# Performance work log

Measured on AMD Instinct MI355X. Metric: run time of the kernel, lower is better.

The kernel has to match this reference:

```python
import jax, jax.numpy as jnp
import numpy as np

N = 1_000_000   # gaussians
K_NB = 10       # neighbor control points per gaussian
K_TOTAL = 300   # num_fine control points


def _normalize(q, eps=1e-8):
    return q / jnp.maximum(jnp.linalg.norm(q, axis=-1, keepdims=True), eps)


def quaternion_to_rotation_matrix(q):
    # q: [..., 4] in (w, x, y, z); normalized before conversion
    q = _normalize(q)
    w, x, y, z = q[..., 0], q[..., 1], q[..., 2], q[..., 3]
    R = jnp.stack([
        jnp.stack([1 - 2 * (y * y + z * z), 2 * (x * y - w * z), 2 * (x * z + w * y)], axis=-1),
        jnp.stack([2 * (x * y + w * z), 1 - 2 * (x * x + z * z), 2 * (y * z - w * x)], axis=-1),
        jnp.stack([2 * (x * z - w * y), 2 * (y * z + w * x), 1 - 2 * (x * x + y * y)], axis=-1),
    ], axis=-2)  # [..., 3, 3]
    return R


def quaternion_multiply(a, b):
    # Hamilton product, (w, x, y, z)
    aw, ax, ay, az = a[..., 0], a[..., 1], a[..., 2], a[..., 3]
    bw, bx, by, bz = b[..., 0], b[..., 1], b[..., 2], b[..., 3]
    return jnp.stack([
        aw * bw - ax * bx - ay * by - az * bz,
        aw * bx + ax * bw + ay * bz - az * by,
        aw * by - ax * bz + ay * bw + az * bx,
        aw * bz + ax * by - ay * bx + az * bw,
    ], axis=-1)


def setup_inputs() -> dict:
    key = jax.random.key(0)
    ks = jax.random.split(key, 7)
    means = jax.random.normal(ks[0], (N, 3), dtype=jnp.float32)
    quaternions = _normalize(jax.random.normal(ks[1], (N, 4), dtype=jnp.float32))
    w = jax.random.uniform(ks[2], (N, K_NB), dtype=jnp.float32) + 1e-3
    weights = w / w.sum(-1, keepdims=True)  # blending weights sum to 1
    indices = jax.random.randint(ks[3], (N, K_NB), 0, K_TOTAL)
    ctrl_translations = 0.1 * jax.random.normal(ks[4], (K_TOTAL, 3), dtype=jnp.float32)
    ctrl_rotations = _normalize(jax.random.normal(ks[5], (K_TOTAL, 4), dtype=jnp.float32))
    ctrl_positions = jax.random.normal(ks[6], (K_TOTAL, 3), dtype=jnp.float32)
    return {
        'means': means, 'quaternions': quaternions, 'weights': weights,
        'ctrl_translations': ctrl_translations, 'ctrl_rotations': ctrl_rotations,
        'ctrl_positions': ctrl_positions, 'indices': indices,
    }


def reference(means, quaternions, weights, ctrl_translations, ctrl_rotations, ctrl_positions, indices):
    # gather neighbor control-point transforms
    nb_trans = ctrl_translations[indices]   # [N, K, 3]
    nb_rots = ctrl_rotations[indices]       # [N, K, 4]
    nb_pos = ctrl_positions[indices]        # [N, K, 3]

    diff = means[:, None, :] - nb_pos                       # [N, K, 3]
    R_ctrl = quaternion_to_rotation_matrix(nb_rots)         # [N, K, 3, 3]
    rotated_diff = jnp.einsum('nkij,nkj->nki', R_ctrl, diff)
    deformed_per_cp = rotated_diff + nb_pos + nb_trans      # [N, K, 3]

    w = weights[..., None]                                  # [N, K, 1]
    deformed_means = (w * deformed_per_cp).sum(axis=1)      # [N, 3]

    blended_rot = _normalize((w * nb_rots).sum(axis=1))     # [N, 4]
    deformed_quats = quaternion_multiply(blended_rot, quaternions)
    return deformed_means, deformed_quats
```

## Files before the change

### kernel.cpp

```cpp
#include <hip/hip_runtime.h>
#include <math.h>


struct Accum {
    float W;
    float Mxx, Myy, Mzz, Mxy, Mxz, Myz, Mwx, Mwy, Mwz;
    float qsw, qsx, qsy, qsz;
    float bsx, bsy, bsz;
};

__device__ __forceinline__ void acc_init(Accum& a) {
    a.W = 0.0f;
    a.Mxx = a.Myy = a.Mzz = 0.0f;
    a.Mxy = a.Mxz = a.Myz = 0.0f;
    a.Mwx = a.Mwy = a.Mwz = 0.0f;
    a.qsw = a.qsx = a.qsy = a.qsz = 0.0f;
    a.bsx = a.bsy = a.bsz = 0.0f;
}

__device__ __forceinline__ void acc_neighbor(Accum& a, const float4* __restrict__ tbl,
                                             int K_TOTAL, int cp, float w) {
    float4 q = tbl[cp];
    float4 b = tbl[K_TOTAL + cp];
    float tw = w * q.x, tx = w * q.y, ty = w * q.z, tz = w * q.w;
    a.W += w;
    a.Mxx = fmaf(tx, q.y, a.Mxx);
    a.Myy = fmaf(ty, q.z, a.Myy);
    a.Mzz = fmaf(tz, q.w, a.Mzz);
    a.Mxy = fmaf(tx, q.z, a.Mxy);
    a.Mxz = fmaf(tx, q.w, a.Mxz);
    a.Myz = fmaf(ty, q.w, a.Myz);
    a.Mwx = fmaf(tw, q.y, a.Mwx);
    a.Mwy = fmaf(tw, q.z, a.Mwy);
    a.Mwz = fmaf(tw, q.w, a.Mwz);
    a.qsw += tw; a.qsx += tx; a.qsy += ty; a.qsz += tz;
    a.bsx = fmaf(w, b.x, a.bsx);
    a.bsy = fmaf(w, b.y, a.bsy);
    a.bsz = fmaf(w, b.z, a.bsz);
}

__device__ __forceinline__ void acc_epilogue(const Accum& a,
                                             float mx, float my, float mz,
                                             float4 g,
                                             float* dmx, float* dmy, float* dmz,
                                             float4* oq) {
    float A00 = a.W - 2.0f * (a.Myy + a.Mzz);
    float A01 = 2.0f * (a.Mxy - a.Mwz);
    float A02 = 2.0f * (a.Mxz + a.Mwy);
    float A10 = 2.0f * (a.Mxy + a.Mwz);
    float A11 = a.W - 2.0f * (a.Mxx + a.Mzz);
    float A12 = 2.0f * (a.Myz - a.Mwx);
    float A20 = 2.0f * (a.Mxz - a.Mwy);
    float A21 = 2.0f * (a.Myz + a.Mwx);
    float A22 = a.W - 2.0f * (a.Mxx + a.Myy);

    *dmx = fmaf(A00, mx, fmaf(A01, my, fmaf(A02, mz, a.bsx)));
    *dmy = fmaf(A10, mx, fmaf(A11, my, fmaf(A12, mz, a.bsy)));
    *dmz = fmaf(A20, mx, fmaf(A21, my, fmaf(A22, mz, a.bsz)));

    float n   = sqrtf(a.qsw * a.qsw + a.qsx * a.qsx + a.qsy * a.qsy + a.qsz * a.qsz);
    float inv = 1.0f / fmaxf(n, 1e-8f);
    float bw = a.qsw * inv, bx = a.qsx * inv, by = a.qsy * inv, bz = a.qsz * inv;

    float gw = g.x, gx = g.y, gy = g.z, gz = g.w;
    oq->x = bw * gw - bx * gx - by * gy - bz * gz;
    oq->y = bw * gx + bx * gw + by * gz - bz * gy;
    oq->z = bw * gy - bx * gz + by * gw + bz * gx;
    oq->w = bw * gz + bx * gy - by * gx + bz * gw;
}

__device__ __forceinline__ void build_table(
    const float* __restrict__ ctrl_trans,
    const float* __restrict__ ctrl_rot,
    const float* __restrict__ ctrl_pos,
    float4* __restrict__ tbl, int K_TOTAL)
{
    for (int cp = threadIdx.x; cp < K_TOTAL; cp += blockDim.x) {
        float4 qv = ((const float4*)ctrl_rot)[cp];
        float qw = qv.x, qx = qv.y, qy = qv.z, qz = qv.w;
        float nn  = sqrtf(qw * qw + qx * qx + qy * qy + qz * qz);
        float inv = 1.0f / fmaxf(nn, 1e-8f);
        float w = qw * inv, x = qx * inv, y = qy * inv, z = qz * inv;
        float R00 = 1.0f - 2.0f * (y * y + z * z);
        float R01 = 2.0f * (x * y - w * z);
        float R02 = 2.0f * (x * z + w * y);
        float R10 = 2.0f * (x * y + w * z);
        float R11 = 1.0f - 2.0f * (x * x + z * z);
        float R12 = 2.0f * (y * z - w * x);
        float R20 = 2.0f * (x * z - w * y);
        float R21 = 2.0f * (y * z + w * x);
        float R22 = 1.0f - 2.0f * (x * x + y * y);
        float px = ctrl_pos[cp * 3 + 0];
        float py = ctrl_pos[cp * 3 + 1];
        float pz = ctrl_pos[cp * 3 + 2];
        float tx = ctrl_trans[cp * 3 + 0];
        float ty = ctrl_trans[cp * 3 + 1];
        float tz = ctrl_trans[cp * 3 + 2];
        tbl[cp]           = make_float4(w, x, y, z);
        tbl[K_TOTAL + cp] = make_float4(px + tx - (R00 * px + R01 * py + R02 * pz),
                                        py + ty - (R10 * px + R11 * py + R12 * pz),
                                        pz + tz - (R20 * px + R21 * py + R22 * pz),
                                        0.0f);
    }
}

__global__ __launch_bounds__(256) void deform_stage_kernel(
    const float* __restrict__ means,
    const float* __restrict__ quats,
    const float* __restrict__ weights,
    const float* __restrict__ ctrl_trans,
    const float* __restrict__ ctrl_rot,
    const float* __restrict__ ctrl_pos,
    const int*   __restrict__ indices,
    float* __restrict__ out_means,
    float* __restrict__ out_quats,
    int N, int K_TOTAL)
{
    extern __shared__ float smem[];
    float4* tbl  = (float4*)smem;
    float*  sIdx = smem + 8 * K_TOTAL;
    float*  sW   = sIdx + 2560;

    const int t = threadIdx.x;
    const long long blockBase = (long long)blockIdx.x * 256;
    const long long fbase = blockBase * 10;
    const long long ftot  = (long long)N * 10;

#pragma unroll
    for (int j = t; j < 640; j += 256) {
        long long f0 = fbase + 4LL * j;
        float4 vi, vw;
        if (f0 + 3 < ftot) {
            vi = ((const float4*)indices)[f0 / 4];
            vw = ((const float4*)weights)[f0 / 4];
        } else {
            float ei[4], ew[4];
#pragma unroll
            for (int e = 0; e < 4; e++) {
                long long f = f0 + e;
                bool ok = f < ftot;
                ei[e] = ok ? ((const float*)indices)[f] : 0.0f;
                ew[e] = ok ? weights[f] : 0.0f;
            }
            vi = make_float4(ei[0], ei[1], ei[2], ei[3]);
            vw = make_float4(ew[0], ew[1], ew[2], ew[3]);
        }
        *(float4*)(sIdx + 4 * j) = vi;
        *(float4*)(sW   + 4 * j) = vw;
    }

    build_table(ctrl_trans, ctrl_rot, ctrl_pos, tbl, K_TOTAL);

    __syncthreads();

    long long g = blockBase + t;
    if (g >= N) return;

    const int2*   ip2 = (const int2*)  (sIdx + t * 10);
    const float2* wp2 = (const float2*)(sW   + t * 10);
    int2   i01 = ip2[0], i23 = ip2[1], i45 = ip2[2], i67 = ip2[3], i89 = ip2[4];
    float2 w01 = wp2[0], w23 = wp2[1], w45 = wp2[2], w67 = wp2[3], w89 = wp2[4];

    float mx = means[g * 3 + 0];
    float my = means[g * 3 + 1];
    float mz = means[g * 3 + 2];
    float4 gq = ((const float4*)quats)[g];

    Accum a; acc_init(a);
    acc_neighbor(a, tbl, K_TOTAL, i01.x, w01.x);
    acc_neighbor(a, tbl, K_TOTAL, i01.y, w01.y);
    acc_neighbor(a, tbl, K_TOTAL, i23.x, w23.x);
    acc_neighbor(a, tbl, K_TOTAL, i23.y, w23.y);
    acc_neighbor(a, tbl, K_TOTAL, i45.x, w45.x);
    acc_neighbor(a, tbl, K_TOTAL, i45.y, w45.y);
    acc_neighbor(a, tbl, K_TOTAL, i67.x, w67.x);
    acc_neighbor(a, tbl, K_TOTAL, i67.y, w67.y);
    acc_neighbor(a, tbl, K_TOTAL, i89.x, w89.x);
    acc_neighbor(a, tbl, K_TOTAL, i89.y, w89.y);

    float dx, dy, dz;
    float4 oq;
    acc_epilogue(a, mx, my, mz, gq, &dx, &dy, &dz, &oq);

    out_means[g * 3 + 0] = dx;
    out_means[g * 3 + 1] = dy;
    out_means[g * 3 + 2] = dz;
    ((float4*)out_quats)[g] = oq;
}

__global__ __launch_bounds__(256) void deform_generic_kernel(
    const float* __restrict__ means,
    const float* __restrict__ quats,
    const float* __restrict__ weights,
    const float* __restrict__ ctrl_trans,
    const float* __restrict__ ctrl_rot,
    const float* __restrict__ ctrl_pos,
    const int*   __restrict__ indices,
    float* __restrict__ out_means,
    float* __restrict__ out_quats,
    int N, int K_NB, int K_TOTAL)
{
    extern __shared__ float smem[];
    float4* tbl = (float4*)smem;
    build_table(ctrl_trans, ctrl_rot, ctrl_pos, tbl, K_TOTAL);
    __syncthreads();

    long long i = (long long)blockIdx.x * blockDim.x + threadIdx.x;
    if (i >= N) return;

    const int*   idx_row = indices + i * K_NB;
    const float* w_row   = weights + i * K_NB;
    Accum a; acc_init(a);
    for (int k = 0; k < K_NB; k++)
        acc_neighbor(a, tbl, K_TOTAL, idx_row[k], w_row[k]);

    float mx = means[i * 3 + 0];
    float my = means[i * 3 + 1];
    float mz = means[i * 3 + 2];
    float4 gq = ((const float4*)quats)[i];
    float dx, dy, dz;
    float4 oq;
    acc_epilogue(a, mx, my, mz, gq, &dx, &dy, &dz, &oq);
    out_means[i * 3 + 0] = dx;
    out_means[i * 3 + 1] = dy;
    out_means[i * 3 + 2] = dz;
    ((float4*)out_quats)[i] = oq;
}

extern "C" void kernel_launch(void* const* d_in, const int* in_sizes, int n_in,
                              void* d_out, int out_size, void* d_ws, size_t ws_size,
                              hipStream_t stream) {
    const float* means      = (const float*)d_in[0];
    const float* quats      = (const float*)d_in[1];
    const float* weights    = (const float*)d_in[2];
    const float* ctrl_trans = (const float*)d_in[3];
    const float* ctrl_rot   = (const float*)d_in[4];
    const float* ctrl_pos   = (const float*)d_in[5];
    const int*   indices    = (const int*)d_in[6];

    int N       = in_sizes[0] / 3;
    int K_NB    = in_sizes[2] / N;
    int K_TOTAL = in_sizes[3] / 3;

    float* out_means = (float*)d_out;
    float* out_quats = (float*)d_out + (long long)N * 3;

    int block = 256;
    int grid  = (int)(((long long)N + block - 1) / block);

    if (K_NB == 10) {
        size_t smem = (size_t)(8 * K_TOTAL + 5120) * sizeof(float);
        deform_stage_kernel<<<grid, block, smem, stream>>>(
            means, quats, weights, ctrl_trans, ctrl_rot, ctrl_pos, indices,
            out_means, out_quats, N, K_TOTAL);
    } else {
        size_t smem = (size_t)K_TOTAL * 2 * sizeof(float4);
        deform_generic_kernel<<<grid, block, smem, stream>>>(
            means, quats, weights, ctrl_trans, ctrl_rot, ctrl_pos, indices,
            out_means, out_quats, N, K_NB, K_TOTAL);
    }
}
```

Before: 148.8 us.

## Replace smem-staged kernel with persistent grid-stride kernel and register prefetch

Replaces the per-block kernel that staged indices and weights through shared memory with a persistent grid-stride kernel capped at 1024 blocks. Each thread loads the next element's indices, weights, mean and quaternion into registers while it processes the current one. The control-point table is now built once per persistent block instead of once per 256 elements. The trade-offs are uncoalesced strided loads of indices and weights (40-byte rows per thread), higher register pressure from the double-buffered data, and a grid size that may not give enough waves in flight.

```diff
diff --git a/kernel.cpp b/kernel.cpp
--- a/kernel.cpp
+++ b/kernel.cpp
@@ -104,7 +104,57 @@
     }
 }
 
-__global__ __launch_bounds__(256) void deform_stage_kernel(
+struct GData {
+    int2   i01, i23, i45, i67, i89;
+    float2 w01, w23, w45, w67, w89;
+    float  mx, my, mz;
+    float4 gq;
+};
+
+__device__ __forceinline__ void load_g(
+    const float* __restrict__ means,
+    const float* __restrict__ quats,
+    const float* __restrict__ weights,
+    const int*   __restrict__ indices,
+    long long g, GData& d)
+{
+    const int2*   ip = (const int2*)(indices + g * 10);
+    const float2* wp = (const float2*)(weights + g * 10);
+    d.i01 = ip[0]; d.i23 = ip[1]; d.i45 = ip[2]; d.i67 = ip[3]; d.i89 = ip[4];
+    d.w01 = wp[0]; d.w23 = wp[1]; d.w45 = wp[2]; d.w67 = wp[3]; d.w89 = wp[4];
+    d.mx = means[g * 3 + 0];
+    d.my = means[g * 3 + 1];
+    d.mz = means[g * 3 + 2];
+    d.gq = ((const float4*)quats)[g];
+}
+
+__device__ __forceinline__ void process_g(
+    const float4* __restrict__ tbl, int K_TOTAL, const GData& d,
+    long long g, float* __restrict__ out_means, float* __restrict__ out_quats)
+{
+    Accum a; acc_init(a);
+    acc_neighbor(a, tbl, K_TOTAL, d.i01.x, d.w01.x);
+    acc_neighbor(a, tbl, K_TOTAL, d.i01.y, d.w01.y);
+    acc_neighbor(a, tbl, K_TOTAL, d.i23.x, d.w23.x);
+    acc_neighbor(a, tbl, K_TOTAL, d.i23.y, d.w23.y);
+    acc_neighbor(a, tbl, K_TOTAL, d.i45.x, d.w45.x);
+    acc_neighbor(a, tbl, K_TOTAL, d.i45.y, d.w45.y);
+    acc_neighbor(a, tbl, K_TOTAL, d.i67.x, d.w67.x);
+    acc_neighbor(a, tbl, K_TOTAL, d.i67.y, d.w67.y);
+    acc_neighbor(a, tbl, K_TOTAL, d.i89.x, d.w89.x);
+    acc_neighbor(a, tbl, K_TOTAL, d.i89.y, d.w89.y);
+
+    float dx, dy, dz;
+    float4 oq;
+    acc_epilogue(a, d.mx, d.my, d.mz, d.gq, &dx, &dy, &dz, &oq);
+
+    out_means[g * 3 + 0] = dx;
+    out_means[g * 3 + 1] = dy;
+    out_means[g * 3 + 2] = dz;
+    ((float4*)out_quats)[g] = oq;
+}
+
+__global__ __launch_bounds__(256) void deform_pipe_kernel(
     const float* __restrict__ means,
     const float* __restrict__ quats,
     const float* __restrict__ weights,
@@ -116,76 +166,32 @@
     float* __restrict__ out_quats,
     int N, int K_TOTAL)
 {
-    extern __shared__ float smem[];
-    float4* tbl  = (float4*)smem;
-    float*  sIdx = smem + 8 * K_TOTAL;
-    float*  sW   = sIdx + 2560;
-
-    const int t = threadIdx.x;
-    const long long blockBase = (long long)blockIdx.x * 256;
-    const long long fbase = blockBase * 10;
-    const long long ftot  = (long long)N * 10;
-
-#pragma unroll
-    for (int j = t; j < 640; j += 256) {
-        long long f0 = fbase + 4LL * j;
-        float4 vi, vw;
-        if (f0 + 3 < ftot) {
-            vi = ((const float4*)indices)[f0 / 4];
-            vw = ((const float4*)weights)[f0 / 4];
-        } else {
-            float ei[4], ew[4];
-#pragma unroll
-            for (int e = 0; e < 4; e++) {
-                long long f = f0 + e;
-                bool ok = f < ftot;
-                ei[e] = ok ? ((const float*)indices)[f] : 0.0f;
-                ew[e] = ok ? weights[f] : 0.0f;
-            }
-            vi = make_float4(ei[0], ei[1], ei[2], ei[3]);
-            vw = make_float4(ew[0], ew[1], ew[2], ew[3]);
+    extern __shared__ float4 tbl[];
+    build_table(ctrl_trans, ctrl_rot, ctrl_pos, tbl, K_TOTAL);
+    __syncthreads();
+
+    const long long stride = (long long)gridDim.x * blockDim.x;
+    long long g = (long long)blockIdx.x * blockDim.x + threadIdx.x;
+    if (g >= N) return;
+
+    GData cur;
+    load_g(means, quats, weights, indices, g, cur);
+
+    for (;;) {
+        long long gn = g + stride;
+        bool have_next = gn < N;
+
+        GData nxt;
+        if (have_next) {
+            load_g(means, quats, weights, indices, gn, nxt);
         }
-        *(float4*)(sIdx + 4 * j) = vi;
-        *(float4*)(sW   + 4 * j) = vw;
+
+        process_g(tbl, K_TOTAL, cur, g, out_means, out_quats);
+
+        if (!have_next) break;
+        cur = nxt;
+        g = gn;
     }
-
-    build_table(ctrl_trans, ctrl_rot, ctrl_pos, tbl, K_TOTAL);
-
-    __syncthreads();
-
-    long long g = blockBase + t;
-    if (g >= N) return;
-
-    const int2*   ip2 = (const int2*)  (sIdx + t * 10);
-    const float2* wp2 = (const float2*)(sW   + t * 10);
-    int2   i01 = ip2[0], i23 = ip2[1], i45 = ip2[2], i67 = ip2[3], i89 = ip2[4];
-    float2 w01 = wp2[0], w23 = wp2[1], w45 = wp2[2], w67 = wp2[3], w89 = wp2[4];
-
-    float mx = means[g * 3 + 0];
-    float my = means[g * 3 + 1];
-    float mz = means[g * 3 + 2];
-    float4 gq = ((const float4*)quats)[g];
-
-    Accum a; acc_init(a);
-    acc_neighbor(a, tbl, K_TOTAL, i01.x, w01.x);
-    acc_neighbor(a, tbl, K_TOTAL, i01.y, w01.y);
-    acc_neighbor(a, tbl, K_TOTAL, i23.x, w23.x);
-    acc_neighbor(a, tbl, K_TOTAL, i23.y, w23.y);
-    acc_neighbor(a, tbl, K_TOTAL, i45.x, w45.x);
-    acc_neighbor(a, tbl, K_TOTAL, i45.y, w45.y);
-    acc_neighbor(a, tbl, K_TOTAL, i67.x, w67.x);
-    acc_neighbor(a, tbl, K_TOTAL, i67.y, w67.y);
-    acc_neighbor(a, tbl, K_TOTAL, i89.x, w89.x);
-    acc_neighbor(a, tbl, K_TOTAL, i89.y, w89.y);
-
-    float dx, dy, dz;
-    float4 oq;
-    acc_epilogue(a, mx, my, mz, gq, &dx, &dy, &dz, &oq);
-
-    out_means[g * 3 + 0] = dx;
-    out_means[g * 3 + 1] = dy;
-    out_means[g * 3 + 2] = dz;
-    ((float4*)out_quats)[g] = oq;
 }
 
 __global__ __launch_bounds__(256) void deform_generic_kernel(
@@ -200,8 +206,7 @@
     float* __restrict__ out_quats,
     int N, int K_NB, int K_TOTAL)
 {
-    extern __shared__ float smem[];
-    float4* tbl = (float4*)smem;
+    extern __shared__ float4 tbl[];
     build_table(ctrl_trans, ctrl_rot, ctrl_pos, tbl, K_TOTAL);
     __syncthreads();
 
@@ -246,15 +251,16 @@
     float* out_quats = (float*)d_out + (long long)N * 3;
 
     int block = 256;
-    int grid  = (int)(((long long)N + block - 1) / block);
+    size_t smem = (size_t)K_TOTAL * 2 * sizeof(float4);
 
     if (K_NB == 10) {
-        size_t smem = (size_t)(8 * K_TOTAL + 5120) * sizeof(float);
-        deform_stage_kernel<<<grid, block, smem, stream>>>(
+        long long need = ((long long)N + block - 1) / block;
+        int grid = (int)(need < 1024 ? need : 1024);
+        deform_pipe_kernel<<<grid, block, smem, stream>>>(
             means, quats, weights, ctrl_trans, ctrl_rot, ctrl_pos, indices,
             out_means, out_quats, N, K_TOTAL);
     } else {
-        size_t smem = (size_t)K_TOTAL * 2 * sizeof(float4);
+        int grid = (int)(((long long)N + block - 1) / block);
         deform_generic_kernel<<<grid, block, smem, stream>>>(
             means, quats, weights, ctrl_trans, ctrl_rot, ctrl_pos, indices,
             out_means, out_quats, N, K_NB, K_TOTAL);
```

After: 150.6 us. About the same (+1.2%).

## Drop LDS staging of indices/weights and use nontemporal global loads/stores

Applied to the files above, without the earlier changes.

The K=10 kernel no longer stages indices and weights through shared memory with coalesced float4 loads. Each thread now reads its own row directly with 8-byte nontemporal loads, and all outputs are written with nontemporal stores. The aim is to cut LDS footprint, raising occupancy, and to remove the staging pass, while keeping streaming data from polluting the cache. The cost is that per-thread strided row reads (40-byte stride) coalesce less well than the old block-wide float4 loads.

```diff
diff --git a/kernel.cpp b/kernel.cpp
--- a/kernel.cpp
+++ b/kernel.cpp
@@ -1,6 +1,10 @@
 #include <hip/hip_runtime.h>
 #include <math.h>
 
+
+typedef float f32x2 __attribute__((ext_vector_type(2)));
+typedef float f32x4 __attribute__((ext_vector_type(4)));
+typedef int   i32x2 __attribute__((ext_vector_type(2)));
 
 struct Accum {
     float W;
@@ -41,9 +45,9 @@
 
 __device__ __forceinline__ void acc_epilogue(const Accum& a,
                                              float mx, float my, float mz,
-                                             float4 g,
+                                             float gw, float gx, float gy, float gz,
                                              float* dmx, float* dmy, float* dmz,
-                                             float4* oq) {
+                                             f32x4* oq) {
     float A00 = a.W - 2.0f * (a.Myy + a.Mzz);
     float A01 = 2.0f * (a.Mxy - a.Mwz);
     float A02 = 2.0f * (a.Mxz + a.Mwy);
@@ -62,11 +66,12 @@
     float inv = 1.0f / fmaxf(n, 1e-8f);
     float bw = a.qsw * inv, bx = a.qsx * inv, by = a.qsy * inv, bz = a.qsz * inv;
 
-    float gw = g.x, gx = g.y, gy = g.z, gz = g.w;
-    oq->x = bw * gw - bx * gx - by * gy - bz * gz;
-    oq->y = bw * gx + bx * gw + by * gz - bz * gy;
-    oq->z = bw * gy - bx * gz + by * gw + bz * gx;
-    oq->w = bw * gz + bx * gy - by * gx + bz * gw;
+    f32x4 r;
+    r.x = bw * gw - bx * gx - by * gy - bz * gz;
+    r.y = bw * gx + bx * gw + by * gz - bz * gy;
+    r.z = bw * gy - bx * gz + by * gw + bz * gx;
+    r.w = bw * gz + bx * gy - by * gx + bz * gw;
+    *oq = r;
 }
 
 __device__ __forceinline__ void build_table(
@@ -104,7 +109,7 @@
     }
 }
 
-__global__ __launch_bounds__(256) void deform_stage_kernel(
+__global__ __launch_bounds__(256) void deform_nt_kernel(
     const float* __restrict__ means,
     const float* __restrict__ quats,
     const float* __restrict__ weights,
@@ -116,55 +121,30 @@
     float* __restrict__ out_quats,
     int N, int K_TOTAL)
 {
-    extern __shared__ float smem[];
-    float4* tbl  = (float4*)smem;
-    float*  sIdx = smem + 8 * K_TOTAL;
-    float*  sW   = sIdx + 2560;
-
-    const int t = threadIdx.x;
-    const long long blockBase = (long long)blockIdx.x * 256;
-    const long long fbase = blockBase * 10;
-    const long long ftot  = (long long)N * 10;
-
-#pragma unroll
-    for (int j = t; j < 640; j += 256) {
-        long long f0 = fbase + 4LL * j;
-        float4 vi, vw;
-        if (f0 + 3 < ftot) {
-            vi = ((const float4*)indices)[f0 / 4];
-            vw = ((const float4*)weights)[f0 / 4];
-        } else {
-            float ei[4], ew[4];
-#pragma unroll
-            for (int e = 0; e < 4; e++) {
-                long long f = f0 + e;
-                bool ok = f < ftot;
-                ei[e] = ok ? ((const float*)indices)[f] : 0.0f;
-                ew[e] = ok ? weights[f] : 0.0f;
-            }
-            vi = make_float4(ei[0], ei[1], ei[2], ei[3]);
-            vw = make_float4(ew[0], ew[1], ew[2], ew[3]);
-        }
-        *(float4*)(sIdx + 4 * j) = vi;
-        *(float4*)(sW   + 4 * j) = vw;
-    }
-
+    extern __shared__ float4 tbl[];
     build_table(ctrl_trans, ctrl_rot, ctrl_pos, tbl, K_TOTAL);
-
     __syncthreads();
 
-    long long g = blockBase + t;
-    if (g >= N) return;
-
-    const int2*   ip2 = (const int2*)  (sIdx + t * 10);
-    const float2* wp2 = (const float2*)(sW   + t * 10);
-    int2   i01 = ip2[0], i23 = ip2[1], i45 = ip2[2], i67 = ip2[3], i89 = ip2[4];
-    float2 w01 = wp2[0], w23 = wp2[1], w45 = wp2[2], w67 = wp2[3], w89 = wp2[4];
-
-    float mx = means[g * 3 + 0];
-    float my = means[g * 3 + 1];
-    float mz = means[g * 3 + 2];
-    float4 gq = ((const float4*)quats)[g];
+    long long i = (long long)blockIdx.x * blockDim.x + threadIdx.x;
+    if (i >= N) return;
+
+    const i32x2* ip = (const i32x2*)(indices + i * 10);
+    const f32x2* wp = (const f32x2*)(weights + i * 10);
+    i32x2 i01 = __builtin_nontemporal_load(ip + 0);
+    i32x2 i23 = __builtin_nontemporal_load(ip + 1);
+    i32x2 i45 = __builtin_nontemporal_load(ip + 2);
+    i32x2 i67 = __builtin_nontemporal_load(ip + 3);
+    i32x2 i89 = __builtin_nontemporal_load(ip + 4);
+    f32x2 w01 = __builtin_nontemporal_load(wp + 0);
+    f32x2 w23 = __builtin_nontemporal_load(wp + 1);
+    f32x2 w45 = __builtin_nontemporal_load(wp + 2);
+    f32x2 w67 = __builtin_nontemporal_load(wp + 3);
+    f32x2 w89 = __builtin_nontemporal_load(wp + 4);
+
+    float mx = __builtin_nontemporal_load(means + i * 3 + 0);
+    float my = __builtin_nontemporal_load(means + i * 3 + 1);
+    float mz = __builtin_nontemporal_load(means + i * 3 + 2);
+    f32x4 gq = __builtin_nontemporal_load((const f32x4*)quats + i);
 
     Accum a; acc_init(a);
     acc_neighbor(a, tbl, K_TOTAL, i01.x, w01.x);
@@ -179,13 +159,13 @@
     acc_neighbor(a, tbl, K_TOTAL, i89.y, w89.y);
 
     float dx, dy, dz;
-    float4 oq;
-    acc_epilogue(a, mx, my, mz, gq, &dx, &dy, &dz, &oq);
-
-    out_means[g * 3 + 0] = dx;
-    out_means[g * 3 + 1] = dy;
-    out_means[g * 3 + 2] = dz;
-    ((float4*)out_quats)[g] = oq;
+    f32x4 oq;
+    acc_epilogue(a, mx, my, mz, gq.x, gq.y, gq.z, gq.w, &dx, &dy, &dz, &oq);
+
+    __builtin_nontemporal_store(dx, out_means + i * 3 + 0);
+    __builtin_nontemporal_store(dy, out_means + i * 3 + 1);
+    __builtin_nontemporal_store(dz, out_means + i * 3 + 2);
+    __builtin_nontemporal_store(oq, (f32x4*)out_quats + i);
 }
 
 __global__ __launch_bounds__(256) void deform_generic_kernel(
@@ -200,8 +180,7 @@
     float* __restrict__ out_quats,
     int N, int K_NB, int K_TOTAL)
 {
-    extern __shared__ float smem[];
-    float4* tbl = (float4*)smem;
+    extern __shared__ float4 tbl[];
     build_table(ctrl_trans, ctrl_rot, ctrl_pos, tbl, K_TOTAL);
     __syncthreads();
 
@@ -217,14 +196,15 @@
     float mx = means[i * 3 + 0];
     float my = means[i * 3 + 1];
     float mz = means[i * 3 + 2];
-    float4 gq = ((const float4*)quats)[i];
+    float4 g4 = ((const float4*)quats)[i];
     float dx, dy, dz;
-    float4 oq;
-    acc_epilogue(a, mx, my, mz, gq, &dx, &dy, &dz, &oq);
+    f32x4 oq;
+    acc_epilogue(a, mx, my, mz, g4.x, g4.y, g4.z, g4.w, &dx, &dy, &dz, &oq);
     out_means[i * 3 + 0] = dx;
     out_means[i * 3 + 1] = dy;
     out_means[i * 3 + 2] = dz;
-    ((float4*)out_quats)[i] = oq;
+    float4* oqp = (float4*)(out_quats + i * 4);
+    *oqp = make_float4(oq.x, oq.y, oq.z, oq.w);
 }
 
 extern "C" void kernel_launch(void* const* d_in, const int* in_sizes, int n_in,
@@ -247,14 +227,13 @@
 
     int block = 256;
     int grid  = (int)(((long long)N + block - 1) / block);
+    size_t smem = (size_t)K_TOTAL * 2 * sizeof(float4);
 
     if (K_NB == 10) {
-        size_t smem = (size_t)(8 * K_TOTAL + 5120) * sizeof(float);
-        deform_stage_kernel<<<grid, block, smem, stream>>>(
+        deform_nt_kernel<<<grid, block, smem, stream>>>(
             means, quats, weights, ctrl_trans, ctrl_rot, ctrl_pos, indices,
             out_means, out_quats, N, K_TOTAL);
     } else {
-        size_t smem = (size_t)K_TOTAL * 2 * sizeof(float4);
         deform_generic_kernel<<<grid, block, smem, stream>>>(
             means, quats, weights, ctrl_trans, ctrl_rot, ctrl_pos, indices,
             out_means, out_quats, N, K_NB, K_TOTAL);
```

Result: slower. 159.5 us (+7.3%).
